# Kernel tuning notes

Hardware: AMD Instinct MI355X
Metric: run time of the kernel (lower is better)

## Reference

```python
import jax, jax.numpy as jnp
import numpy as np

B, S, D, H = 2, 4096, 512, 8
HD = D // H

def setup_inputs() -> dict:
    key = jax.random.key(0)
    ks = jax.random.split(key, 9)
    s = 1.0 / np.sqrt(D)
    inp = {"x": jax.random.normal(ks[0], (B, S, D), dtype=jnp.float32)}
    names = ["Wq", "Wk", "Wv", "Wo"]
    for i, n in enumerate(names):
        inp[n] = jax.random.uniform(ks[1 + 2 * i], (D, D), jnp.float32, -s, s)
        inp["b" + n[1]] = jax.random.uniform(ks[2 + 2 * i], (D,), jnp.float32, -s, s)
    return inp


def reference(x, Wq, bq, Wk, bk, Wv, bv, Wo, bo):
    # projections (torch Linear: x @ W.T + b)
    def proj(W, b):
        return (x @ W.T + b).reshape(B, S, H, HD).transpose(0, 2, 1, 3)  # [B,H,S,HD]
    q = proj(Wq, bq)
    k = proj(Wk, bk)
    v = proj(Wv, bv)
    scores = jnp.einsum("bhqd,bhkd->bhqk", q, k) / np.sqrt(HD).astype(np.float32)
    attn = jax.nn.softmax(scores, axis=-1)
    out = jnp.einsum("bhqk,bhkd->bhqd", attn, v)
    out = out.transpose(0, 2, 1, 3).reshape(B, S, D)
    return out @ Wo.T + bo
```

## Files before the change

kernel.cpp:

```cpp
#include <hip/hip_runtime.h>
#include <hip/hip_bf16.h>

#define DEV __device__ __forceinline__

typedef float f32x4 __attribute__((ext_vector_type(4)));
typedef float f32x16 __attribute__((ext_vector_type(16)));
typedef __bf16 bf16x8 __attribute__((ext_vector_type(8)));
typedef unsigned short u16;
typedef unsigned short u16x8 __attribute__((ext_vector_type(8)));

DEV u16 f2bf(float f) {
    __bf16 h = (__bf16)f;
    return __builtin_bit_cast(u16, h);
}

DEV f32x4 mfma16(bf16x8 a, bf16x8 b, f32x4 c) {
    return __builtin_amdgcn_mfma_f32_16x16x32_bf16(a, b, c, 0, 0, 0);
}
DEV f32x16 mfma32(bf16x8 a, bf16x8 b, f32x16 c) {
    return __builtin_amdgcn_mfma_f32_32x32x16_bf16(a, b, c, 0, 0, 0);
}

DEV unsigned cvtpk(float lo, float hi) {
    unsigned r;
    asm("v_cvt_pk_bf16_f32 %0, %1, %2" : "=v"(r) : "v"(lo), "v"(hi));
    return r;
}
DEV void pswap(unsigned& a, unsigned& b) {
    asm volatile("v_permlane32_swap_b32 %0, %1" : "+v"(a), "+v"(b));
}

DEV int kidx(int row, int col) { return row * 64 + (col ^ ((row & 7) << 3)); }
DEV int xidx(int row, int col) { return row * 32 + (col ^ ((row & 3) << 3)); }

__global__ __launch_bounds__(256) void cvt_kernel(
    const float* __restrict__ x, const float* __restrict__ wq,
    const float* __restrict__ wk, const float* __restrict__ wv,
    const float* __restrict__ wo,
    u16* __restrict__ xb, u16* __restrict__ wb)
{
    size_t e0 = ((size_t)blockIdx.x * 256 + threadIdx.x) * 8;
    const float* src; u16* dst; size_t off;
    if (e0 < 4194304) { src = x; dst = xb; off = e0; }
    else {
        size_t r = e0 - 4194304;
        int seg = (int)(r >> 18);
        src = (seg == 0) ? wq : (seg == 1) ? wk : (seg == 2) ? wv : wo;
        dst = wb + (size_t)seg * 262144;
        off = r & 262143;
    }
    f32x4 a = *(const f32x4*)(src + off);
    f32x4 b = *(const f32x4*)(src + off + 4);
    u16x8 o;
    #pragma unroll
    for (int i = 0; i < 4; ++i) { o[i] = f2bf(a[i]); o[i + 4] = f2bf(b[i]); }
    *(u16x8*)(dst + off) = o;
}

__global__ __launch_bounds__(256) void proj_qkv_kernel(
    const u16* __restrict__ xb, const u16* __restrict__ wb,
    const float* __restrict__ bq, const float* __restrict__ bk, const float* __restrict__ bv,
    u16* __restrict__ qo, u16* __restrict__ ko, u16* __restrict__ vo)
{
    __shared__ u16 Xs[128 * 32], Wsh[128 * 32];
    const int tid = threadIdx.x;
    const int m0 = blockIdx.x * 128, n0 = blockIdx.y * 128, z = blockIdx.z;
    const u16* W = wb + (size_t)z * 262144;
    const float* bias = (z == 0) ? bq : (z == 1) ? bk : bv;

    const int lane = tid & 63, wv = tid >> 6;
    const int g = lane >> 4, c = lane & 15;
    const int wr = wv >> 1, wcl = wv & 1;
    const int srow = tid >> 1, scol = (tid & 1) * 16;

    f32x4 acc[4][4] = {};

    for (int k0 = 0; k0 < 512; k0 += 32) {
        const u16* xp = xb + (size_t)(m0 + srow) * 512 + k0 + scol;
        const u16* wp = W  + (size_t)(n0 + srow) * 512 + k0 + scol;
        uint4 xa = *(const uint4*)xp, xa2 = *(const uint4*)(xp + 8);
        uint4 wa = *(const uint4*)wp, wa2 = *(const uint4*)(wp + 8);
        __syncthreads();
        *(uint4*)&Xs[xidx(srow, scol)]      = xa;
        *(uint4*)&Xs[xidx(srow, scol + 8)]  = xa2;
        *(uint4*)&Wsh[xidx(srow, scol)]     = wa;
        *(uint4*)&Wsh[xidx(srow, scol + 8)] = wa2;
        __syncthreads();

        bf16x8 af[4], bfr[4];
        #pragma unroll
        for (int mt = 0; mt < 4; ++mt)
            af[mt] = *(const bf16x8*)&Xs[xidx(wr * 64 + mt * 16 + c, g * 8)];
        #pragma unroll
        for (int nt = 0; nt < 4; ++nt)
            bfr[nt] = *(const bf16x8*)&Wsh[xidx(wcl * 64 + nt * 16 + c, g * 8)];

        if (z < 2) {
            #pragma unroll
            for (int mt = 0; mt < 4; ++mt)
                #pragma unroll
                for (int nt = 0; nt < 4; ++nt)
                    acc[mt][nt] = mfma16(af[mt], bfr[nt], acc[mt][nt]);
        } else {
            #pragma unroll
            for (int mt = 0; mt < 4; ++mt)
                #pragma unroll
                for (int nt = 0; nt < 4; ++nt)
                    acc[mt][nt] = mfma16(bfr[nt], af[mt], acc[mt][nt]);
        }
    }

    if (z < 2) {
        const float scale = (z == 0) ? 0.18033688011112042f : 1.0f;
        u16* outp = (z == 0) ? qo : ko;
        float bn[4];
        #pragma unroll
        for (int nt = 0; nt < 4; ++nt) bn[nt] = bias[n0 + wcl * 64 + nt * 16 + c];
        #pragma unroll
        for (int mt = 0; mt < 4; ++mt)
            #pragma unroll
            for (int r = 0; r < 4; ++r) {
                int mg = m0 + wr * 64 + mt * 16 + g * 4 + r;
                int b = mg >> 12, s = mg & 4095;
                #pragma unroll
                for (int nt = 0; nt < 4; ++nt) {
                    int ng = n0 + wcl * 64 + nt * 16 + c;
                    int h = ng >> 6, d = ng & 63;
                    outp[((size_t)(b * 8 + h) * 4096 + s) * 64 + d] =
                        f2bf((acc[mt][nt][r] + bn[nt]) * scale);
                }
            }
    } else {
        #pragma unroll
        for (int nt = 0; nt < 4; ++nt)
            #pragma unroll
            for (int r = 0; r < 4; ++r) {
                int ng = n0 + wcl * 64 + nt * 16 + g * 4 + r;
                int h = ng >> 6, d = ng & 63;
                float bnr = bias[ng];
                #pragma unroll
                for (int mt = 0; mt < 4; ++mt) {
                    int mg = m0 + wr * 64 + mt * 16 + c;
                    int b = mg >> 12, s = mg & 4095;
                    vo[((size_t)(b * 8 + h) * 64 + d) * 4096 + s] =
                        f2bf(acc[mt][nt][r] + bnr);
                }
            }
    }
}

__global__ __launch_bounds__(256) void flash_attn_kernel(
    const u16* __restrict__ Q, const u16* __restrict__ K,
    const u16* __restrict__ Vt, u16* __restrict__ O)
{
    __shared__ u16 Ks[2][64 * 64];
    __shared__ u16 Vs[2][64 * 64];

    const int tid = threadIdx.x;
    const int bh = blockIdx.y;
    const int q0 = blockIdx.x * 128;
    const int lane = tid & 63, wv = tid >> 6;
    const int l31 = lane & 31, hi = lane >> 5;

    const u16* Qb = Q  + (size_t)bh * (4096 * 64);
    const u16* Kb = K  + (size_t)bh * (4096 * 64);
    const u16* Vb = Vt + (size_t)bh * (64 * 4096);

    const int qrow = q0 + wv * 32 + l31;
    bf16x8 qf[4];
    #pragma unroll
    for (int ds = 0; ds < 4; ++ds)
        qf[ds] = *(const bf16x8*)(Qb + (size_t)qrow * 64 + ds * 16 + hi * 8);

    f32x16 oA[2] = {};
    float l_ = 0.f;

    const int sr = tid >> 3, sc8 = (tid & 7) * 8;
    const u16* kp0 = Kb + (size_t)sr * 64 + sc8;
    const u16* vp0 = Vb + (size_t)sr * 4096 + sc8;

    uint4 rk0 = *(const uint4*)(kp0);
    uint4 rk1 = *(const uint4*)(kp0 + 32 * 64);
    uint4 rv0 = *(const uint4*)(vp0);
    uint4 rv1 = *(const uint4*)(vp0 + 32 * 4096);

    for (int t = 0; t < 64; ++t) {
        const int p = t & 1;
        *(uint4*)&Ks[p][kidx(sr, sc8)]      = rk0;
        *(uint4*)&Ks[p][kidx(sr + 32, sc8)] = rk1;
        *(uint4*)&Vs[p][kidx(sr, sc8)]      = rv0;
        *(uint4*)&Vs[p][kidx(sr + 32, sc8)] = rv1;
        if (t < 63) {
            const int kv1 = (t + 1) * 64;
            rk0 = *(const uint4*)(kp0 + (size_t)kv1 * 64);
            rk1 = *(const uint4*)(kp0 + (size_t)(kv1 + 32) * 64);
            rv0 = *(const uint4*)(vp0 + kv1);
            rv1 = *(const uint4*)(vp0 + 32 * 4096 + kv1);
        }
        __syncthreads();

        f32x16 sA0 = {}, sA1 = {};
        #pragma unroll
        for (int ds = 0; ds < 4; ++ds) {
            bf16x8 kf0 = *(const bf16x8*)&Ks[p][kidx(l31,      ds * 16 + hi * 8)];
            bf16x8 kf1 = *(const bf16x8*)&Ks[p][kidx(32 + l31, ds * 16 + hi * 8)];
            sA0 = mfma32(kf0, qf[ds], sA0);
            sA1 = mfma32(kf1, qf[ds], sA1);
        }

        bf16x8 pf[4];
        #pragma unroll
        for (int ct = 0; ct < 2; ++ct) {
            const f32x16 sA = ct ? sA1 : sA0;
            float pv[16];
            #pragma unroll
            for (int r = 0; r < 16; ++r) {
                pv[r] = __builtin_amdgcn_exp2f(sA[r]);
                l_ += pv[r];
            }
            unsigned a0 = cvtpk(pv[0],  pv[1]),  a1 = cvtpk(pv[2],  pv[3]);
            unsigned b0 = cvtpk(pv[4],  pv[5]),  b1 = cvtpk(pv[6],  pv[7]);
            pswap(a0, b0); pswap(a1, b1);
            uint4 w0; w0.x = a0; w0.y = a1; w0.z = b0; w0.w = b1;
            pf[2 * ct] = __builtin_bit_cast(bf16x8, w0);
            unsigned c0 = cvtpk(pv[8],  pv[9]),  c1 = cvtpk(pv[10], pv[11]);
            unsigned d0 = cvtpk(pv[12], pv[13]), d1 = cvtpk(pv[14], pv[15]);
            pswap(c0, d0); pswap(c1, d1);
            uint4 w1; w1.x = c0; w1.y = c1; w1.z = d0; w1.w = d1;
            pf[2 * ct + 1] = __builtin_bit_cast(bf16x8, w1);
        }

        #pragma unroll
        for (int ks = 0; ks < 4; ++ks) {
            bf16x8 vf0 = *(const bf16x8*)&Vs[p][kidx(l31,      ks * 16 + hi * 8)];
            bf16x8 vf1 = *(const bf16x8*)&Vs[p][kidx(32 + l31, ks * 16 + hi * 8)];
            oA[0] = mfma32(vf0, pf[ks], oA[0]);
            oA[1] = mfma32(vf1, pf[ks], oA[1]);
        }
    }

    l_ += __shfl_xor(l_, 32);
    const float inv = 1.0f / l_;

    const int b = bh >> 3, h = bh & 7;
    u16* Ob = O + ((size_t)(b * 4096 + qrow)) * 512 + h * 64;
    #pragma unroll
    for (int dt = 0; dt < 2; ++dt) {
        const f32x16 oa = dt ? oA[1] : oA[0];
        #pragma unroll
        for (int qd = 0; qd < 4; ++qd) {
            unsigned w0 = cvtpk(oa[qd * 4 + 0] * inv, oa[qd * 4 + 1] * inv);
            unsigned w1 = cvtpk(oa[qd * 4 + 2] * inv, oa[qd * 4 + 3] * inv);
            uint2 st; st.x = w0; st.y = w1;
            *(uint2*)(Ob + dt * 32 + qd * 8 + hi * 4) = st;
        }
    }
}

__global__ __launch_bounds__(256) void out_proj_kernel(
    const u16* __restrict__ Ob, const u16* __restrict__ Wob,
    const float* __restrict__ bo, float* __restrict__ out)
{
    __shared__ u16 Xs[128 * 32], Wsh[128 * 32];
    const int tid = threadIdx.x;
    const int m0 = blockIdx.x * 128, n0 = blockIdx.y * 128;

    const int lane = tid & 63, wv = tid >> 6;
    const int g = lane >> 4, c = lane & 15;
    const int wr = wv >> 1, wcl = wv & 1;
    const int srow = tid >> 1, scol = (tid & 1) * 16;

    f32x4 acc[4][4] = {};

    for (int k0 = 0; k0 < 512; k0 += 32) {
        const u16* xp = Ob  + (size_t)(m0 + srow) * 512 + k0 + scol;
        const u16* wp = Wob + (size_t)(n0 + srow) * 512 + k0 + scol;
        uint4 xa = *(const uint4*)xp, xa2 = *(const uint4*)(xp + 8);
        uint4 wa = *(const uint4*)wp, wa2 = *(const uint4*)(wp + 8);
        __syncthreads();
        *(uint4*)&Xs[xidx(srow, scol)]      = xa;
        *(uint4*)&Xs[xidx(srow, scol + 8)]  = xa2;
        *(uint4*)&Wsh[xidx(srow, scol)]     = wa;
        *(uint4*)&Wsh[xidx(srow, scol + 8)] = wa2;
        __syncthreads();

        bf16x8 af[4], bfr[4];
        #pragma unroll
        for (int mt = 0; mt < 4; ++mt)
            af[mt] = *(const bf16x8*)&Xs[xidx(wr * 64 + mt * 16 + c, g * 8)];
        #pragma unroll
        for (int nt = 0; nt < 4; ++nt)
            bfr[nt] = *(const bf16x8*)&Wsh[xidx(wcl * 64 + nt * 16 + c, g * 8)];

        #pragma unroll
        for (int mt = 0; mt < 4; ++mt)
            #pragma unroll
            for (int nt = 0; nt < 4; ++nt)
                acc[mt][nt] = mfma16(bfr[nt], af[mt], acc[mt][nt]);
    }

    #pragma unroll
    for (int nt = 0; nt < 4; ++nt) {
        f32x4 bi = *(const f32x4*)&bo[n0 + wcl * 64 + nt * 16 + g * 4];
        #pragma unroll
        for (int mt = 0; mt < 4; ++mt) {
            int m = m0 + wr * 64 + mt * 16 + c;
            f32x4 v;
            #pragma unroll
            for (int r = 0; r < 4; ++r) v[r] = acc[mt][nt][r] + bi[r];
            *(f32x4*)&out[(size_t)m * 512 + n0 + wcl * 64 + nt * 16 + g * 4] = v;
        }
    }
}

extern "C" void kernel_launch(void* const* d_in, const int* in_sizes, int n_in,
                              void* d_out, int out_size, void* d_ws, size_t ws_size,
                              hipStream_t stream) {
    const float* x  = (const float*)d_in[0];
    const float* Wq = (const float*)d_in[1];
    const float* bq = (const float*)d_in[2];
    const float* Wk = (const float*)d_in[3];
    const float* bk = (const float*)d_in[4];
    const float* Wv = (const float*)d_in[5];
    const float* bv = (const float*)d_in[6];
    const float* Wo = (const float*)d_in[7];
    const float* bo = (const float*)d_in[8];
    float* out = (float*)d_out;

    const size_t NQKV = (size_t)2 * 8 * 4096 * 64;
    u16* qw = (u16*)d_ws;
    u16* kw = qw + NQKV;
    u16* vw = kw + NQKV;
    u16* wbuf = vw + NQKV;
    u16* rbuf = wbuf + 4 * 262144;
    u16* xbuf = rbuf;
    u16* obuf = rbuf;

    cvt_kernel<<<2560, 256, 0, stream>>>(x, Wq, Wk, Wv, Wo, xbuf, wbuf);
    proj_qkv_kernel<<<dim3(64, 4, 3), 256, 0, stream>>>(xbuf, wbuf, bq, bk, bv, qw, kw, vw);
    flash_attn_kernel<<<dim3(32, 16), 256, 0, stream>>>(qw, kw, vw, obuf);
    out_proj_kernel<<<dim3(64, 4), 256, 0, stream>>>(obuf, wbuf + 3 * 262144, bo, out);
}
```

Baseline: 150.3 us.

## Split attention over KV halves with combine kernel and fuse x conversion into projection

Flash attention now runs each query tile over two KV halves in separate blocks, writing unnormalized bf16 partial outputs and row sums. A new combine kernel adds the halves and normalizes them. This doubles the block count to improve CU occupancy. The x fp32-to-bf16 conversion moves into the QKV projection loads, removing a pass over x. The costs are an extra kernel and partial-output traffic through the output buffer, plus bf16 rounding of the partial sums.

```diff
diff --git a/kernel.cpp b/kernel.cpp
--- a/kernel.cpp
+++ b/kernel.cpp
@@ -13,6 +13,10 @@
     __bf16 h = (__bf16)f;
     return __builtin_bit_cast(u16, h);
 }
+DEV float bf2f(u16 u) {
+    __bf16 h = __builtin_bit_cast(__bf16, u);
+    return (float)h;
+}
 
 DEV f32x4 mfma16(bf16x8 a, bf16x8 b, f32x4 c) {
     return __builtin_amdgcn_mfma_f32_16x16x32_bf16(a, b, c, 0, 0, 0);
@@ -34,21 +38,15 @@
 DEV int xidx(int row, int col) { return row * 32 + (col ^ ((row & 3) << 3)); }
 
 __global__ __launch_bounds__(256) void cvt_kernel(
-    const float* __restrict__ x, const float* __restrict__ wq,
-    const float* __restrict__ wk, const float* __restrict__ wv,
-    const float* __restrict__ wo,
-    u16* __restrict__ xb, u16* __restrict__ wb)
+    const float* __restrict__ wq, const float* __restrict__ wk,
+    const float* __restrict__ wv, const float* __restrict__ wo,
+    u16* __restrict__ wb)
 {
     size_t e0 = ((size_t)blockIdx.x * 256 + threadIdx.x) * 8;
-    const float* src; u16* dst; size_t off;
-    if (e0 < 4194304) { src = x; dst = xb; off = e0; }
-    else {
-        size_t r = e0 - 4194304;
-        int seg = (int)(r >> 18);
-        src = (seg == 0) ? wq : (seg == 1) ? wk : (seg == 2) ? wv : wo;
-        dst = wb + (size_t)seg * 262144;
-        off = r & 262143;
-    }
+    int seg = (int)(e0 >> 18);
+    const float* src = (seg == 0) ? wq : (seg == 1) ? wk : (seg == 2) ? wv : wo;
+    u16* dst = wb + (size_t)seg * 262144;
+    size_t off = e0 & 262143;
     f32x4 a = *(const f32x4*)(src + off);
     f32x4 b = *(const f32x4*)(src + off + 4);
     u16x8 o;
@@ -58,7 +56,7 @@
 }
 
 __global__ __launch_bounds__(256) void proj_qkv_kernel(
-    const u16* __restrict__ xb, const u16* __restrict__ wb,
+    const float* __restrict__ x, const u16* __restrict__ wb,
     const float* __restrict__ bq, const float* __restrict__ bk, const float* __restrict__ bv,
     u16* __restrict__ qo, u16* __restrict__ ko, u16* __restrict__ vo)
 {
@@ -76,13 +74,20 @@
     f32x4 acc[4][4] = {};
 
     for (int k0 = 0; k0 < 512; k0 += 32) {
-        const u16* xp = xb + (size_t)(m0 + srow) * 512 + k0 + scol;
-        const u16* wp = W  + (size_t)(n0 + srow) * 512 + k0 + scol;
-        uint4 xa = *(const uint4*)xp, xa2 = *(const uint4*)(xp + 8);
+        const float* xp = x + (size_t)(m0 + srow) * 512 + k0 + scol;
+        const u16* wp = W + (size_t)(n0 + srow) * 512 + k0 + scol;
+        f32x4 xa = *(const f32x4*)xp,       xb2 = *(const f32x4*)(xp + 4);
+        f32x4 xc = *(const f32x4*)(xp + 8), xd  = *(const f32x4*)(xp + 12);
         uint4 wa = *(const uint4*)wp, wa2 = *(const uint4*)(wp + 8);
         __syncthreads();
-        *(uint4*)&Xs[xidx(srow, scol)]      = xa;
-        *(uint4*)&Xs[xidx(srow, scol + 8)]  = xa2;
+        u16x8 px0, px1;
+        #pragma unroll
+        for (int j = 0; j < 4; ++j) {
+            px0[j] = f2bf(xa[j]); px0[j + 4] = f2bf(xb2[j]);
+            px1[j] = f2bf(xc[j]); px1[j + 4] = f2bf(xd[j]);
+        }
+        *(u16x8*)&Xs[xidx(srow, scol)]      = px0;
+        *(u16x8*)&Xs[xidx(srow, scol + 8)]  = px1;
         *(uint4*)&Wsh[xidx(srow, scol)]     = wa;
         *(uint4*)&Wsh[xidx(srow, scol + 8)] = wa2;
         __syncthreads();
@@ -151,7 +156,7 @@
 
 __global__ __launch_bounds__(256) void flash_attn_kernel(
     const u16* __restrict__ Q, const u16* __restrict__ K,
-    const u16* __restrict__ Vt, u16* __restrict__ O)
+    const u16* __restrict__ Vt, u16* __restrict__ Opart, float* __restrict__ lbuf)
 {
     __shared__ u16 Ks[2][64 * 64];
     __shared__ u16 Vs[2][64 * 64];
@@ -159,6 +164,8 @@
     const int tid = threadIdx.x;
     const int bh = blockIdx.y;
     const int q0 = blockIdx.x * 128;
+    const int half = blockIdx.z;
+    const int kvbase = half * 2048;
     const int lane = tid & 63, wv = tid >> 6;
     const int l31 = lane & 31, hi = lane >> 5;
 
@@ -176,21 +183,21 @@
     float l_ = 0.f;
 
     const int sr = tid >> 3, sc8 = (tid & 7) * 8;
-    const u16* kp0 = Kb + (size_t)sr * 64 + sc8;
-    const u16* vp0 = Vb + (size_t)sr * 4096 + sc8;
+    const u16* kp0 = Kb + (size_t)(kvbase + sr) * 64 + sc8;
+    const u16* vp0 = Vb + (size_t)sr * 4096 + kvbase + sc8;
 
     uint4 rk0 = *(const uint4*)(kp0);
     uint4 rk1 = *(const uint4*)(kp0 + 32 * 64);
     uint4 rv0 = *(const uint4*)(vp0);
     uint4 rv1 = *(const uint4*)(vp0 + 32 * 4096);
 
-    for (int t = 0; t < 64; ++t) {
+    for (int t = 0; t < 32; ++t) {
         const int p = t & 1;
         *(uint4*)&Ks[p][kidx(sr, sc8)]      = rk0;
         *(uint4*)&Ks[p][kidx(sr + 32, sc8)] = rk1;
         *(uint4*)&Vs[p][kidx(sr, sc8)]      = rv0;
         *(uint4*)&Vs[p][kidx(sr + 32, sc8)] = rv1;
-        if (t < 63) {
+        if (t < 31) {
             const int kv1 = (t + 1) * 64;
             rk0 = *(const uint4*)(kp0 + (size_t)kv1 * 64);
             rk1 = *(const uint4*)(kp0 + (size_t)(kv1 + 32) * 64);
@@ -214,10 +221,11 @@
             const f32x16 sA = ct ? sA1 : sA0;
             float pv[16];
             #pragma unroll
-            for (int r = 0; r < 16; ++r) {
+            for (int r = 0; r < 16; ++r)
                 pv[r] = __builtin_amdgcn_exp2f(sA[r]);
-                l_ += pv[r];
-            }
+            #pragma unroll
+            for (int r = 0; r < 16; r += 4)
+                l_ += (pv[r] + pv[r + 1]) + (pv[r + 2] + pv[r + 3]);
             unsigned a0 = cvtpk(pv[0],  pv[1]),  a1 = cvtpk(pv[2],  pv[3]);
             unsigned b0 = cvtpk(pv[4],  pv[5]),  b1 = cvtpk(pv[6],  pv[7]);
             pswap(a0, b0); pswap(a1, b1);
@@ -239,22 +247,45 @@
         }
     }
 
-    l_ += __shfl_xor(l_, 32);
-    const float inv = 1.0f / l_;
+    float l_full = l_ + __shfl_xor(l_, 32);
+    if (hi == 0)
+        lbuf[(size_t)(half * 16 + bh) * 4096 + qrow] = l_full;
 
     const int b = bh >> 3, h = bh & 7;
-    u16* Ob = O + ((size_t)(b * 4096 + qrow)) * 512 + h * 64;
+    u16* Ob = Opart + (size_t)half * 4194304 +
+              ((size_t)(b * 4096 + qrow)) * 512 + h * 64;
     #pragma unroll
     for (int dt = 0; dt < 2; ++dt) {
         const f32x16 oa = dt ? oA[1] : oA[0];
         #pragma unroll
         for (int qd = 0; qd < 4; ++qd) {
-            unsigned w0 = cvtpk(oa[qd * 4 + 0] * inv, oa[qd * 4 + 1] * inv);
-            unsigned w1 = cvtpk(oa[qd * 4 + 2] * inv, oa[qd * 4 + 3] * inv);
+            unsigned w0 = cvtpk(oa[qd * 4 + 0], oa[qd * 4 + 1]);
+            unsigned w1 = cvtpk(oa[qd * 4 + 2], oa[qd * 4 + 3]);
             uint2 st; st.x = w0; st.y = w1;
             *(uint2*)(Ob + dt * 32 + qd * 8 + hi * 4) = st;
         }
     }
+}
+
+__global__ __launch_bounds__(256) void combine_kernel(
+    const u16* __restrict__ Opart, const float* __restrict__ lbuf,
+    u16* __restrict__ obuf)
+{
+    const size_t idx8 = ((size_t)blockIdx.x * 256 + threadIdx.x) * 8;
+    const int m = (int)(idx8 >> 9);
+    const int hd = (int)(idx8 & 511);
+    const int b = m >> 12, s = m & 4095, h = hd >> 6;
+    const int bh = b * 8 + h;
+    const float la = lbuf[(size_t)bh * 4096 + s];
+    const float lb = lbuf[(size_t)(16 + bh) * 4096 + s];
+    const float inv = 1.0f / (la + lb);
+    u16x8 a = *(const u16x8*)(Opart + idx8);
+    u16x8 c = *(const u16x8*)(Opart + 4194304 + idx8);
+    u16x8 o;
+    #pragma unroll
+    for (int i = 0; i < 8; ++i)
+        o[i] = f2bf((bf2f(a[i]) + bf2f(c[i])) * inv);
+    *(u16x8*)(obuf + idx8) = o;
 }
 
 __global__ __launch_bounds__(256) void out_proj_kernel(
@@ -332,12 +363,13 @@
     u16* kw = qw + NQKV;
     u16* vw = kw + NQKV;
     u16* wbuf = vw + NQKV;
-    u16* rbuf = wbuf + 4 * 262144;
-    u16* xbuf = rbuf;
-    u16* obuf = rbuf;
-
-    cvt_kernel<<<2560, 256, 0, stream>>>(x, Wq, Wk, Wv, Wo, xbuf, wbuf);
-    proj_qkv_kernel<<<dim3(64, 4, 3), 256, 0, stream>>>(xbuf, wbuf, bq, bk, bv, qw, kw, vw);
-    flash_attn_kernel<<<dim3(32, 16), 256, 0, stream>>>(qw, kw, vw, obuf);
+    float* lbuf = (float*)(wbuf + 4 * 262144);
+    u16* opart = (u16*)d_out;
+    u16* obuf = qw;
+
+    cvt_kernel<<<512, 256, 0, stream>>>(Wq, Wk, Wv, Wo, wbuf);
+    proj_qkv_kernel<<<dim3(64, 4, 3), 256, 0, stream>>>(x, wbuf, bq, bk, bv, qw, kw, vw);
+    flash_attn_kernel<<<dim3(32, 16, 2), 256, 0, stream>>>(qw, kw, vw, opart, lbuf);
+    combine_kernel<<<2048, 256, 0, stream>>>(opart, lbuf, obuf);
     out_proj_kernel<<<dim3(64, 4), 256, 0, stream>>>(obuf, wbuf + 3 * 262144, bo, out);
 }
```

After: 173.2 us. 15.2% more time.
